# Optimization experiments

Hardware: AMD Instinct MI355X
Metric: run time of the kernel (lower is better)

## Reference

```python
import jax, jax.numpy as jnp
import numpy as np

NFEAT, NHID = 128, 128

def setup_inputs() -> dict:
    key = jax.random.key(0)
    k1, k2, k3, k4 = jax.random.split(key, 4)
    x = jax.random.normal(k1, (32, 1024, NFEAT), dtype=jnp.float32)
    adj = jax.random.uniform(k2, (32, 1024, 1024), dtype=jnp.float32)
    # GraphConvolution parameters (Kipf init ~ uniform, scale irrelevant for correctness)
    bound = 1.0 / np.sqrt(NHID)
    W = jax.random.uniform(k3, (NFEAT, NHID), dtype=jnp.float32, minval=-bound, maxval=bound)
    b = jax.random.uniform(k4, (NHID,), dtype=jnp.float32, minval=-bound, maxval=bound)
    return {"x": x, "adj": adj, "W": W, "b": b}

def reference(x, adj, W, b):
    # Batched equivalent of the per-sample python loop:
    # out[i] = relu(adj[i] @ (x[i] @ W) + b); dropout is identity in eval mode.
    support = jnp.einsum('bnf,fh->bnh', x, W)          # [B, N, nhid]
    out = jnp.einsum('bnm,bmh->bnh', adj, support) + b  # [B, N, nhid]
    return jax.nn.relu(out)
```

## Files before the change

kernel.cpp:

```cpp
#include <hip/hip_runtime.h>
#include <stdint.h>


typedef short bf16x8 __attribute__((ext_vector_type(8)));
typedef float f32x4 __attribute__((ext_vector_type(4)));
typedef int i32x4 __attribute__((ext_vector_type(4)));
typedef unsigned short u16x4 __attribute__((ext_vector_type(4)));

__device__ __forceinline__ unsigned short f2bf(float f) {
    uint32_t u = __builtin_bit_cast(uint32_t, f);
    u += 0x7FFFu + ((u >> 16) & 1u);
    return (unsigned short)(u >> 16);
}

__global__ __launch_bounds__(256) void k0_wt(const float* __restrict__ W,
                                             unsigned short* __restrict__ WT) {
    int o = blockIdx.x * 256 + threadIdx.x;
    int h = o >> 7, f = o & 127;
    WT[o] = f2bf(W[f * 128 + h]);
}

#define K1S 136
__global__ __launch_bounds__(256) void k1_support(const float* __restrict__ x,
                                                  const unsigned short* __restrict__ WT,
                                                  unsigned short* __restrict__ ST) {
    __shared__ __align__(16) unsigned short xt[64 * K1S];
    __shared__ __align__(16) unsigned short wt[128 * K1S];
    int t = threadIdx.x;
    int node_base = blockIdx.x * 64;

    const f32x4* xg = (const f32x4*)(x + (size_t)node_base * 128);
#pragma unroll
    for (int i = 0; i < 8; ++i) {
        int f4 = i * 256 + t;
        int row = f4 >> 5, c4 = f4 & 31;
        f32x4 v = xg[f4];
        u16x4 p;
        p.x = f2bf(v.x); p.y = f2bf(v.y); p.z = f2bf(v.z); p.w = f2bf(v.w);
        *(u16x4*)&xt[row * K1S + c4 * 4] = p;
    }
    const i32x4* wg = (const i32x4*)WT;
#pragma unroll
    for (int i = 0; i < 8; ++i) {
        int c = i * 256 + t;
        int row = c >> 4, ch = c & 15;
        *(i32x4*)&wt[row * K1S + ch * 8] = wg[c];
    }
    __syncthreads();

    int wv = t >> 6, lane = t & 63, l16 = lane & 15, quad = lane >> 4;
    int wave_h = (wv & 1) * 64, wave_m = (wv >> 1) * 32;

    f32x4 acc[4][2];
#pragma unroll
    for (int ht = 0; ht < 4; ++ht)
#pragma unroll
        for (int mt = 0; mt < 2; ++mt) acc[ht][mt] = 0.f;

#pragma unroll
    for (int s = 0; s < 4; ++s) {
        int ko = s * 32 + quad * 8;
        bf16x8 a[4], bb[2];
#pragma unroll
        for (int ht = 0; ht < 4; ++ht)
            a[ht] = *(const bf16x8*)&wt[(wave_h + ht * 16 + l16) * K1S + ko];
#pragma unroll
        for (int mt = 0; mt < 2; ++mt)
            bb[mt] = *(const bf16x8*)&xt[(wave_m + mt * 16 + l16) * K1S + ko];
#pragma unroll
        for (int ht = 0; ht < 4; ++ht)
#pragma unroll
            for (int mt = 0; mt < 2; ++mt)
                acc[ht][mt] = __builtin_amdgcn_mfma_f32_16x16x32_bf16(
                    a[ht], bb[mt], acc[ht][mt], 0, 0, 0);
    }

    int batch = blockIdx.x >> 4;
    int m_in_b = (blockIdx.x & 15) * 64;
#pragma unroll
    for (int ht = 0; ht < 4; ++ht)
#pragma unroll
        for (int mt = 0; mt < 2; ++mt) {
            int mcol = wave_m + mt * 16 + l16;
#pragma unroll
            for (int r = 0; r < 4; ++r) {
                int h = wave_h + ht * 16 + quad * 4 + r;
                ST[(((size_t)batch * 128 + h) << 10) + m_in_b + mcol] =
                    f2bf(acc[ht][mt][r]);
            }
        }
}

#define K2S 72
__global__ __launch_bounds__(256) void k2_gcn(const float* __restrict__ adj,
                                              const unsigned short* __restrict__ ST,
                                              const float* __restrict__ bias,
                                              float* __restrict__ out) {
    __shared__ __align__(16) unsigned short As[64 * K2S];
    __shared__ __align__(16) unsigned short Bs[128 * K2S];
    int t = threadIdx.x;
    int batch = blockIdx.x >> 4;
    int mbase = (blockIdx.x & 15) * 64;
    int wv = t >> 6, lane = t & 63, l16 = lane & 15, quad = lane >> 4;
    int wave_m = (wv & 1) * 32, wave_n = (wv >> 1) * 64;

    float bv[4];
#pragma unroll
    for (int j = 0; j < 4; ++j) bv[j] = bias[wave_n + j * 16 + l16];

    f32x4 acc[2][4];
#pragma unroll
    for (int i = 0; i < 2; ++i)
#pragma unroll
        for (int j = 0; j < 4; ++j) acc[i][j] = 0.f;

    const float* adjb = adj + ((size_t)batch * 1024 + mbase) * 1024;
    const unsigned short* stb = ST + ((size_t)batch * 128) * 1024;

    for (int kb = 0; kb < 16; ++kb) {
#pragma unroll
        for (int i = 0; i < 4; ++i) {
            int f4 = i * 256 + t;
            int row = f4 >> 4, c4 = f4 & 15;
            f32x4 v = *(const f32x4*)(adjb + (size_t)row * 1024 + kb * 64 + c4 * 4);
            u16x4 p;
            p.x = f2bf(v.x); p.y = f2bf(v.y); p.z = f2bf(v.z); p.w = f2bf(v.w);
            *(u16x4*)&As[row * K2S + c4 * 4] = p;
        }
#pragma unroll
        for (int i = 0; i < 4; ++i) {
            int c = i * 256 + t;
            int row = c >> 3, ch = c & 7;
            *(i32x4*)&Bs[row * K2S + ch * 8] =
                *(const i32x4*)(stb + (size_t)row * 1024 + kb * 64 + ch * 8);
        }
        __syncthreads();
#pragma unroll
        for (int s = 0; s < 2; ++s) {
            int ko = s * 32 + quad * 8;
            bf16x8 a[2], bb[4];
#pragma unroll
            for (int i = 0; i < 2; ++i)
                a[i] = *(const bf16x8*)&As[(wave_m + i * 16 + l16) * K2S + ko];
#pragma unroll
            for (int j = 0; j < 4; ++j)
                bb[j] = *(const bf16x8*)&Bs[(wave_n + j * 16 + l16) * K2S + ko];
#pragma unroll
            for (int i = 0; i < 2; ++i)
#pragma unroll
                for (int j = 0; j < 4; ++j)
                    acc[i][j] = __builtin_amdgcn_mfma_f32_16x16x32_bf16(
                        a[i], bb[j], acc[i][j], 0, 0, 0);
        }
        __syncthreads();
    }

    float* outb = out + ((size_t)batch * 1024 + mbase) * 128;
#pragma unroll
    for (int i = 0; i < 2; ++i)
#pragma unroll
        for (int j = 0; j < 4; ++j) {
            int n = wave_n + j * 16 + l16;
#pragma unroll
            for (int r = 0; r < 4; ++r) {
                int m = wave_m + i * 16 + quad * 4 + r;
                float v = acc[i][j][r] + bv[j];
                outb[(size_t)m * 128 + n] = fmaxf(v, 0.f);
            }
        }
}

extern "C" void kernel_launch(void* const* d_in, const int* in_sizes, int n_in,
                              void* d_out, int out_size, void* d_ws, size_t ws_size,
                              hipStream_t stream) {
    const float* x = (const float*)d_in[0];
    const float* adj = (const float*)d_in[1];
    const float* W = (const float*)d_in[2];
    const float* b = (const float*)d_in[3];
    float* out = (float*)d_out;

    unsigned short* ST = (unsigned short*)d_ws;
    unsigned short* WT = (unsigned short*)d_ws + (size_t)32 * 128 * 1024;

    k0_wt<<<64, 256, 0, stream>>>(W, WT);
    k1_support<<<512, 256, 0, stream>>>(x, WT, ST);
    k2_gcn<<<512, 256, 0, stream>>>(adj, ST, b, out);
}
```

Baseline: 224.3 us.

## Double-buffer LDS tiles and prefetch next adj/support tile into registers

```diff
diff --git a/kernel.cpp b/kernel.cpp
--- a/kernel.cpp
+++ b/kernel.cpp
@@ -96,8 +96,8 @@
                                               const unsigned short* __restrict__ ST,
                                               const float* __restrict__ bias,
                                               float* __restrict__ out) {
-    __shared__ __align__(16) unsigned short As[64 * K2S];
-    __shared__ __align__(16) unsigned short Bs[128 * K2S];
+    __shared__ __align__(16) unsigned short As[2][64 * K2S];
+    __shared__ __align__(16) unsigned short Bs[2][128 * K2S];
     int t = threadIdx.x;
     int batch = blockIdx.x >> 4;
     int mbase = (blockIdx.x & 15) * 64;
@@ -117,34 +117,54 @@
     const float* adjb = adj + ((size_t)batch * 1024 + mbase) * 1024;
     const unsigned short* stb = ST + ((size_t)batch * 128) * 1024;
 
+    f32x4 av[4];
+    i32x4 sv[4];
+
+    auto stage_load = [&](int kb) {
+#pragma unroll
+        for (int i = 0; i < 4; ++i) {
+            int row = i * 16 + (t >> 4), c4 = t & 15;
+            av[i] = *(const f32x4*)(adjb + (size_t)row * 1024 + kb * 64 + c4 * 4);
+        }
+#pragma unroll
+        for (int i = 0; i < 4; ++i) {
+            int row = i * 32 + (t >> 3), ch = t & 7;
+            sv[i] = *(const i32x4*)(stb + (size_t)row * 1024 + kb * 64 + ch * 8);
+        }
+    };
+    auto stage_write = [&](int buf) {
+#pragma unroll
+        for (int i = 0; i < 4; ++i) {
+            int row = i * 16 + (t >> 4), c4 = t & 15;
+            u16x4 p;
+            p.x = f2bf(av[i].x); p.y = f2bf(av[i].y);
+            p.z = f2bf(av[i].z); p.w = f2bf(av[i].w);
+            *(u16x4*)&As[buf][row * K2S + c4 * 4] = p;
+        }
+#pragma unroll
+        for (int i = 0; i < 4; ++i) {
+            int row = i * 32 + (t >> 3), ch = t & 7;
+            *(i32x4*)&Bs[buf][row * K2S + ch * 8] = sv[i];
+        }
+    };
+
+    stage_load(0);
+    stage_write(0);
+    __syncthreads();
+
     for (int kb = 0; kb < 16; ++kb) {
-#pragma unroll
-        for (int i = 0; i < 4; ++i) {
-            int f4 = i * 256 + t;
-            int row = f4 >> 4, c4 = f4 & 15;
-            f32x4 v = *(const f32x4*)(adjb + (size_t)row * 1024 + kb * 64 + c4 * 4);
-            u16x4 p;
-            p.x = f2bf(v.x); p.y = f2bf(v.y); p.z = f2bf(v.z); p.w = f2bf(v.w);
-            *(u16x4*)&As[row * K2S + c4 * 4] = p;
-        }
-#pragma unroll
-        for (int i = 0; i < 4; ++i) {
-            int c = i * 256 + t;
-            int row = c >> 3, ch = c & 7;
-            *(i32x4*)&Bs[row * K2S + ch * 8] =
-                *(const i32x4*)(stb + (size_t)row * 1024 + kb * 64 + ch * 8);
-        }
-        __syncthreads();
+        int cur = kb & 1;
+        if (kb < 15) stage_load(kb + 1);
 #pragma unroll
         for (int s = 0; s < 2; ++s) {
             int ko = s * 32 + quad * 8;
             bf16x8 a[2], bb[4];
 #pragma unroll
             for (int i = 0; i < 2; ++i)
-                a[i] = *(const bf16x8*)&As[(wave_m + i * 16 + l16) * K2S + ko];
+                a[i] = *(const bf16x8*)&As[cur][(wave_m + i * 16 + l16) * K2S + ko];
 #pragma unroll
             for (int j = 0; j < 4; ++j)
-                bb[j] = *(const bf16x8*)&Bs[(wave_n + j * 16 + l16) * K2S + ko];
+                bb[j] = *(const bf16x8*)&Bs[cur][(wave_n + j * 16 + l16) * K2S + ko];
 #pragma unroll
             for (int i = 0; i < 2; ++i)
 #pragma unroll
@@ -152,7 +172,10 @@
                     acc[i][j] = __builtin_amdgcn_mfma_f32_16x16x32_bf16(
                         a[i], bb[j], acc[i][j], 0, 0, 0);
         }
-        __syncthreads();
+        if (kb < 15) {
+            stage_write((kb + 1) & 1);
+            __syncthreads();
+        }
     }
 
     float* outb = out + ((size_t)batch * 1024 + mbase) * 128;
```

After: 225.7 us. Within noise of the previous version (+0.6%).

## Drop LDS staging; load MFMA operands directly from global memory

Applied to the files above, without the earlier changes.

```diff
diff --git a/kernel.cpp b/kernel.cpp
--- a/kernel.cpp
+++ b/kernel.cpp
@@ -4,13 +4,19 @@
 
 typedef short bf16x8 __attribute__((ext_vector_type(8)));
 typedef float f32x4 __attribute__((ext_vector_type(4)));
-typedef int i32x4 __attribute__((ext_vector_type(4)));
-typedef unsigned short u16x4 __attribute__((ext_vector_type(4)));
+typedef unsigned short u16x8 __attribute__((ext_vector_type(8)));
 
 __device__ __forceinline__ unsigned short f2bf(float f) {
     uint32_t u = __builtin_bit_cast(uint32_t, f);
     u += 0x7FFFu + ((u >> 16) & 1u);
     return (unsigned short)(u >> 16);
+}
+
+__device__ __forceinline__ bf16x8 cvt8(f32x4 v0, f32x4 v1) {
+    u16x8 p;
+    p[0] = f2bf(v0.x); p[1] = f2bf(v0.y); p[2] = f2bf(v0.z); p[3] = f2bf(v0.w);
+    p[4] = f2bf(v1.x); p[5] = f2bf(v1.y); p[6] = f2bf(v1.z); p[7] = f2bf(v1.w);
+    return __builtin_bit_cast(bf16x8, p);
 }
 
 __global__ __launch_bounds__(256) void k0_wt(const float* __restrict__ W,
@@ -20,36 +26,14 @@
     WT[o] = f2bf(W[f * 128 + h]);
 }
 
-#define K1S 136
 __global__ __launch_bounds__(256) void k1_support(const float* __restrict__ x,
                                                   const unsigned short* __restrict__ WT,
                                                   unsigned short* __restrict__ ST) {
-    __shared__ __align__(16) unsigned short xt[64 * K1S];
-    __shared__ __align__(16) unsigned short wt[128 * K1S];
     int t = threadIdx.x;
-    int node_base = blockIdx.x * 64;
-
-    const f32x4* xg = (const f32x4*)(x + (size_t)node_base * 128);
-#pragma unroll
-    for (int i = 0; i < 8; ++i) {
-        int f4 = i * 256 + t;
-        int row = f4 >> 5, c4 = f4 & 31;
-        f32x4 v = xg[f4];
-        u16x4 p;
-        p.x = f2bf(v.x); p.y = f2bf(v.y); p.z = f2bf(v.z); p.w = f2bf(v.w);
-        *(u16x4*)&xt[row * K1S + c4 * 4] = p;
-    }
-    const i32x4* wg = (const i32x4*)WT;
-#pragma unroll
-    for (int i = 0; i < 8; ++i) {
-        int c = i * 256 + t;
-        int row = c >> 4, ch = c & 15;
-        *(i32x4*)&wt[row * K1S + ch * 8] = wg[c];
-    }
-    __syncthreads();
-
     int wv = t >> 6, lane = t & 63, l16 = lane & 15, quad = lane >> 4;
     int wave_h = (wv & 1) * 64, wave_m = (wv >> 1) * 32;
+    int node_base = blockIdx.x * 64;
+    const float* xb = x + (size_t)node_base * 128;
 
     f32x4 acc[4][2];
 #pragma unroll
@@ -63,10 +47,12 @@
         bf16x8 a[4], bb[2];
 #pragma unroll
         for (int ht = 0; ht < 4; ++ht)
-            a[ht] = *(const bf16x8*)&wt[(wave_h + ht * 16 + l16) * K1S + ko];
+            a[ht] = *(const bf16x8*)&WT[(wave_h + ht * 16 + l16) * 128 + ko];
 #pragma unroll
-        for (int mt = 0; mt < 2; ++mt)
-            bb[mt] = *(const bf16x8*)&xt[(wave_m + mt * 16 + l16) * K1S + ko];
+        for (int mt = 0; mt < 2; ++mt) {
+            const float* xr = xb + (size_t)(wave_m + mt * 16 + l16) * 128 + ko;
+            bb[mt] = cvt8(*(const f32x4*)xr, *(const f32x4*)(xr + 4));
+        }
 #pragma unroll
         for (int ht = 0; ht < 4; ++ht)
 #pragma unroll
@@ -91,13 +77,10 @@
         }
 }
 
-#define K2S 72
 __global__ __launch_bounds__(256) void k2_gcn(const float* __restrict__ adj,
                                               const unsigned short* __restrict__ ST,
                                               const float* __restrict__ bias,
                                               float* __restrict__ out) {
-    __shared__ __align__(16) unsigned short As[64 * K2S];
-    __shared__ __align__(16) unsigned short Bs[128 * K2S];
     int t = threadIdx.x;
     int batch = blockIdx.x >> 4;
     int mbase = (blockIdx.x & 15) * 64;
@@ -119,32 +102,17 @@
 
     for (int kb = 0; kb < 16; ++kb) {
 #pragma unroll
-        for (int i = 0; i < 4; ++i) {
-            int f4 = i * 256 + t;
-            int row = f4 >> 4, c4 = f4 & 15;
-            f32x4 v = *(const f32x4*)(adjb + (size_t)row * 1024 + kb * 64 + c4 * 4);
-            u16x4 p;
-            p.x = f2bf(v.x); p.y = f2bf(v.y); p.z = f2bf(v.z); p.w = f2bf(v.w);
-            *(u16x4*)&As[row * K2S + c4 * 4] = p;
-        }
-#pragma unroll
-        for (int i = 0; i < 4; ++i) {
-            int c = i * 256 + t;
-            int row = c >> 3, ch = c & 7;
-            *(i32x4*)&Bs[row * K2S + ch * 8] =
-                *(const i32x4*)(stb + (size_t)row * 1024 + kb * 64 + ch * 8);
-        }
-        __syncthreads();
-#pragma unroll
         for (int s = 0; s < 2; ++s) {
-            int ko = s * 32 + quad * 8;
+            int ko = kb * 64 + s * 32 + quad * 8;
             bf16x8 a[2], bb[4];
 #pragma unroll
-            for (int i = 0; i < 2; ++i)
-                a[i] = *(const bf16x8*)&As[(wave_m + i * 16 + l16) * K2S + ko];
+            for (int i = 0; i < 2; ++i) {
+                const float* ar = adjb + (size_t)(wave_m + i * 16 + l16) * 1024 + ko;
+                a[i] = cvt8(*(const f32x4*)ar, *(const f32x4*)(ar + 4));
+            }
 #pragma unroll
             for (int j = 0; j < 4; ++j)
-                bb[j] = *(const bf16x8*)&Bs[(wave_n + j * 16 + l16) * K2S + ko];
+                bb[j] = *(const bf16x8*)&stb[(size_t)(wave_n + j * 16 + l16) * 1024 + ko];
 #pragma unroll
             for (int i = 0; i < 2; ++i)
 #pragma unroll
@@ -152,7 +120,6 @@
                     acc[i][j] = __builtin_amdgcn_mfma_f32_16x16x32_bf16(
                         a[i], bb[j], acc[i][j], 0, 0, 0);
         }
-        __syncthreads();
     }
 
     float* outb = out + ((size_t)batch * 1024 + mbase) * 128;
```

Measured after the change: 247.5 us. 1.1x slower.
